# Performance work log

Measured on AMD Instinct MI355X. Metric: run time of the kernel, lower is better.

The kernel has to match this reference:

```python
import jax, jax.numpy as jnp
import numpy as np

B, N, IN_DIM, DIM, HEADS, P = 4, 2048, 256, 512, 8, 16
DH = DIM // HEADS            # 64
SCALE = DH ** -0.5


def setup_inputs() -> dict:
    key = jax.random.key(0)
    ks = jax.random.split(key, 8)
    def w(k, shape, s=0.02):
        return jax.random.normal(k, shape, dtype=jnp.float32) * s
    return {
        "x": jax.random.normal(ks[0], (B, N, IN_DIM), dtype=jnp.float32),
        "w_qkv": w(ks[1], (IN_DIM, 3 * DIM)),
        "b_qkv": jnp.zeros((3 * DIM,), jnp.float32),
        "w_in": w(ks[2], (P, P)),
        "b_in": jnp.zeros((P,), jnp.float32),
        "w_out": w(ks[3], (P, P)),
        "b_out": jnp.zeros((P,), jnp.float32),
        "w_merge": w(ks[4], (DIM, DIM)),
        "b_merge": jnp.zeros((DIM,), jnp.float32),
        "w_proj": w(ks[5], (DIM + IN_DIM, DIM)),
        "b_proj": jnp.zeros((DIM,), jnp.float32),
        "H": 64,
        "W": 32,
    }


def reference(x, w_qkv, b_qkv, w_in, b_in, w_out, b_out,
              w_merge, b_merge, w_proj, b_proj, H, W):
    b, n, _ = x.shape
    qkv = x @ w_qkv + b_qkv                      # [b, n, 3*DIM]
    q, k, v = jnp.split(qkv, 3, axis=-1)
    def to_heads(t):
        return t.reshape(b, n, HEADS, DH).transpose(0, 2, 1, 3)  # [b, h, n, d]
    q, k, v = to_heads(q), to_heads(k), to_heads(v)
    # Original splits heads into h/v halves and runs two attentions, then
    # concats along the head axis. Softmax is per-head, so this is exactly
    # one batched multi-head attention with head order preserved.
    attn = jax.nn.softmax(jnp.einsum('bhnd,bhmd->bhnm', q, k) * SCALE, axis=-1)
    out = jnp.einsum('bhnm,bhmd->bhnd', attn, v)
    out = out.transpose(0, 2, 1, 3).reshape(b, n, DIM)
    out = out @ w_merge + b_merge
    # IBPP branch: view channels as [P, P] grid, linear-SiLU-linear on last dim
    xr = x.reshape(b, n, P, P)
    ib = jax.nn.silu(xr @ w_in + b_in) @ w_out + b_out
    ib = ib.reshape(b, n, IN_DIM)
    # proj (dropout p=0 -> identity)
    return jnp.concatenate([out, ib], axis=-1) @ w_proj + b_proj
```

## Files before the change

### kernel.cpp

```cpp
#include <hip/hip_runtime.h>


typedef unsigned short u16;
typedef unsigned int u32;
typedef __bf16 bf16x8 __attribute__((ext_vector_type(8)));
typedef u16 su16x8 __attribute__((ext_vector_type(8)));
typedef u16 su16x4 __attribute__((ext_vector_type(4)));
typedef u32 u32x4 __attribute__((ext_vector_type(4)));
typedef float f32x4 __attribute__((ext_vector_type(4)));

__device__ __forceinline__ u16 f2bf(float f) {
  union { __bf16 h; u16 u; } v;
  v.h = (__bf16)f;
  return v.u;
}

__device__ __forceinline__ float fexp2(float x) {
#if __has_builtin(__builtin_amdgcn_exp2f)
  return __builtin_amdgcn_exp2f(x);
#else
  return __expf(x * 0.6931471805599453f);
#endif
}

__device__ __forceinline__ f32x4 zero4() {
  f32x4 v = {0.f, 0.f, 0.f, 0.f};
  return v;
}

__device__ __forceinline__ f32x4 mfma16(bf16x8 a, bf16x8 b, f32x4 c) {
  return __builtin_amdgcn_mfma_f32_16x16x32_bf16(a, b, c, 0, 0, 0);
}

__global__ __launch_bounds__(256) void prep_kernel(
    const float* __restrict__ w_qkv, const float* __restrict__ w_merge,
    const float* __restrict__ w_proj, const float* __restrict__ b_merge,
    const float* __restrict__ b_proj, u16* __restrict__ wqkvT,
    u16* __restrict__ wptT, u16* __restrict__ wcombT, u16* __restrict__ wmb,
    float* __restrict__ biasc) {
  int blk = blockIdx.x, tid = threadIdx.x;
  if (blk < 192) {
    const float* src;
    int lsrc, ldd, r0, c0;
    u16* dst;
    if (blk < 96) {
      src = w_qkv; lsrc = 1536; dst = wqkvT; ldd = 256;
      r0 = (blk & 3) * 64; c0 = (blk >> 2) * 64;
    } else if (blk < 160) {
      int b2 = blk - 96;
      src = w_proj; lsrc = 512; dst = wptT; ldd = 512;
      r0 = (b2 & 7) * 64; c0 = (b2 >> 3) * 64;
    } else {
      int b2 = blk - 160;
      src = w_proj + 512 * 512; lsrc = 512; dst = wcombT + 512; ldd = 768;
      r0 = (b2 & 3) * 64; c0 = (b2 >> 2) * 64;
    }
    __shared__ __align__(16) u16 Ts[64 * 68];
    int rr = tid >> 4, cc4 = (tid & 15) * 4;
#pragma unroll
    for (int rep = 0; rep < 4; ++rep) {
      int r = rr + rep * 16;
      float4 v = *(const float4*)&src[(size_t)(r0 + r) * lsrc + c0 + cc4];
      su16x4 pk = {f2bf(v.x), f2bf(v.y), f2bf(v.z), f2bf(v.w)};
      *(su16x4*)&Ts[r * 68 + cc4] = pk;
    }
    __syncthreads();
    int c = tid & 63, seg = tid >> 6;
    u16 tmp[16];
#pragma unroll
    for (int k = 0; k < 16; ++k) tmp[k] = Ts[(seg * 16 + k) * 68 + c];
    *(su16x8*)&dst[(size_t)(c0 + c) * ldd + r0 + seg * 16] = *(su16x8*)tmp;
    *(su16x8*)&dst[(size_t)(c0 + c) * ldd + r0 + seg * 16 + 8] =
        *(su16x8*)(tmp + 8);
  } else if (blk < 256) {
    int b2 = blk - 192;
#pragma unroll
    for (int rep = 0; rep < 4; ++rep) {
      int i = b2 * 4096 + rep * 1024 + tid * 4;
      float4 v = *(const float4*)&w_merge[i];
      su16x4 pk = {f2bf(v.x), f2bf(v.y), f2bf(v.z), f2bf(v.w)};
      *(su16x4*)&wmb[i] = pk;
    }
  } else {
    int col0 = (blk - 256) * 16;
    __shared__ float red[16][17];
    int kr = tid >> 4, cc = tid & 15;
    float s = 0.f;
#pragma unroll 4
    for (int j = 0; j < 32; ++j) {
      int k = kr + j * 16;
      s += b_merge[k] * w_proj[(size_t)k * 512 + col0 + cc];
    }
    red[kr][cc] = s;
    __syncthreads();
    if (kr == 0) {
      float a = b_proj[col0 + cc];
#pragma unroll
      for (int t = 0; t < 16; ++t) a += red[t][cc];
      biasc[col0 + cc] = a;
    }
  }
}

__global__ __launch_bounds__(256) void ib_kernel(
    const float* __restrict__ x, const float* __restrict__ w_in,
    const float* __restrict__ b_in, const float* __restrict__ w_out,
    const float* __restrict__ b_out, u16* __restrict__ xb,
    u16* __restrict__ catb) {
  __shared__ float wi[256], wo[256], bi[16], bo[16];
  __shared__ float xs[16][260];
  __shared__ float hs[16][260];
  int tid = threadIdx.x;
  wi[tid] = w_in[tid];
  wo[tid] = w_out[tid];
  if (tid < 16) { bi[tid] = b_in[tid]; bo[tid] = b_out[tid]; }
  size_t blkoff = (size_t)blockIdx.x * 4096;
#pragma unroll
  for (int i = 0; i < 4; ++i) {
    int f = (tid + i * 256) * 4;
    float4 v = *(const float4*)&x[blkoff + f];
    int tok = f >> 8, p = f & 255;
    *(float4*)&xs[tok][p] = v;
    su16x4 pk = {f2bf(v.x), f2bf(v.y), f2bf(v.z), f2bf(v.w)};
    *(su16x4*)&xb[blkoff + f] = pk;
  }
  __syncthreads();
  int t = tid >> 4, p2 = tid & 15;
#pragma unroll
  for (int p1 = 0; p1 < 16; ++p1) {
    float a = bi[p2];
#pragma unroll
    for (int k = 0; k < 16; ++k) a += xs[t][p1 * 16 + k] * wi[k * 16 + p2];
    hs[t][p1 * 16 + p2] = a / (1.f + __expf(-a));
  }
  __syncthreads();
  size_t tok = (size_t)blockIdx.x * 16 + t;
#pragma unroll
  for (int p1 = 0; p1 < 16; ++p1) {
    float o = bo[p2];
#pragma unroll
    for (int j = 0; j < 16; ++j) o += hs[t][p1 * 16 + j] * wo[j * 16 + p2];
    catb[tok * 768 + 512 + p1 * 16 + p2] = f2bf(o);
  }
}

template <int TM, int TN, int WGM, int WGN, int OUTMODE>
__global__ __launch_bounds__(256) void gemm_bt(
    const u16* __restrict__ A, int lda, const u16* __restrict__ BT, int ldb,
    int kcount, const float* __restrict__ bias, void* __restrict__ Co, int ldc,
    int scaleQ) {
  constexpr int NROWS = TM + TN;
  constexpr int NLD = NROWS / 64;
  constexpr int MT = TM / WGM / 16;
  constexpr int NT = TN / WGN / 16;
  __shared__ __align__(16) u16 S[NROWS * 40];
  int tid = threadIdx.x;
  int lane = tid & 63, wave = tid >> 6;
  int c = lane & 15, g4 = lane >> 4;
  int m0 = blockIdx.y * TM, n0 = blockIdx.x * TN;
  int wm = (wave / WGN) * (TM / WGM), wn = (wave % WGN) * (TN / WGN);
  f32x4 acc[MT][NT];
#pragma unroll
  for (int a = 0; a < MT; ++a)
#pragma unroll
    for (int b = 0; b < NT; ++b) acc[a][b] = zero4();

  su16x8 pre[NLD];
#pragma unroll
  for (int t = 0; t < NLD; ++t) {
    int gsl = t * 256 + tid;
    int row = gsl >> 2, kg = gsl & 3;
    const u16* p = row < TM ? &A[(size_t)(m0 + row) * lda + kg * 8]
                            : &BT[(size_t)(n0 + row - TM) * ldb + kg * 8];
    pre[t] = *(const su16x8*)p;
  }

  for (int kb = 0; kb < kcount; kb += 32) {
    __syncthreads();
#pragma unroll
    for (int t = 0; t < NLD; ++t) {
      int gsl = t * 256 + tid;
      int row = gsl >> 2, kg = gsl & 3;
      *(su16x8*)&S[row * 40 + kg * 8] = pre[t];
    }
    __syncthreads();
    if (kb + 32 < kcount) {
#pragma unroll
      for (int t = 0; t < NLD; ++t) {
        int gsl = t * 256 + tid;
        int row = gsl >> 2, kg = gsl & 3;
        const u16* p =
            row < TM ? &A[(size_t)(m0 + row) * lda + kb + 32 + kg * 8]
                     : &BT[(size_t)(n0 + row - TM) * ldb + kb + 32 + kg * 8];
        pre[t] = *(const su16x8*)p;
      }
    }
    bf16x8 af[MT], bf[NT];
#pragma unroll
    for (int mt = 0; mt < MT; ++mt)
      af[mt] = *(const bf16x8*)&S[(wm + mt * 16 + c) * 40 + g4 * 8];
#pragma unroll
    for (int nt = 0; nt < NT; ++nt)
      bf[nt] = *(const bf16x8*)&S[(TM + wn + nt * 16 + c) * 40 + g4 * 8];
#pragma unroll
    for (int mt = 0; mt < MT; ++mt)
#pragma unroll
      for (int nt = 0; nt < NT; ++nt)
        acc[mt][nt] = mfma16(af[mt], bf[nt], acc[mt][nt]);
  }

  if (OUTMODE == 0) {
    float* Cf = (float*)Co;
#pragma unroll
    for (int nt = 0; nt < NT; ++nt) {
      int col = n0 + wn + nt * 16 + c;
      float bv = bias ? bias[col] : 0.f;
#pragma unroll
      for (int mt = 0; mt < MT; ++mt)
#pragma unroll
        for (int i = 0; i < 4; ++i)
          Cf[(size_t)(m0 + wm + mt * 16 + g4 * 4 + i) * ldc + col] =
              acc[mt][nt][i] + bv;
    }
  } else if (OUTMODE == 2) {
    u16* C16 = (u16*)Co;
#pragma unroll
    for (int nt = 0; nt < NT; ++nt)
#pragma unroll
      for (int mt = 0; mt < MT; ++mt)
#pragma unroll
        for (int i = 0; i < 4; ++i)
          C16[(size_t)(m0 + wm + mt * 16 + g4 * 4 + i) * ldc + n0 + wn +
              nt * 16 + c] = f2bf(acc[mt][nt][i]);
  } else {
    u16* C16 = (u16*)Co;
    u16* Cs = S;
    __syncthreads();
#pragma unroll
    for (int half = 0; half < 2; ++half) {
      if ((wave >> 1) == half) {
#pragma unroll
        for (int nt = 0; nt < NT; ++nt) {
          int col = n0 + wn + nt * 16 + c;
          float bv = bias ? bias[col] : 0.f;
          float sc = (scaleQ && col < 512) ? 0.18033688011112042f : 1.f;
#pragma unroll
          for (int mt = 0; mt < MT; ++mt)
#pragma unroll
            for (int i = 0; i < 4; ++i)
              Cs[(mt * 16 + g4 * 4 + i) * 136 + wn + nt * 16 + c] =
                  f2bf((acc[mt][nt][i] + bv) * sc);
        }
      }
      __syncthreads();
      {
        int row = tid >> 2;
#pragma unroll
        for (int t = 0; t < 4; ++t) {
          int gr = (tid & 3) + t * 4;
          u32x4 v = *(const u32x4*)&Cs[row * 136 + gr * 8];
          *(u32x4*)&C16[(size_t)(m0 + half * 64 + row) * ldc + n0 + gr * 8] = v;
        }
      }
      __syncthreads();
    }
  }
}

__global__ __launch_bounds__(256) void attn_kernel(
    const u16* __restrict__ qkvb, u16* __restrict__ catb) {
  __shared__ __align__(16) u16 Ks[9216];
  __shared__ __align__(16) u16 Vs[8704];
  __shared__ __align__(16) u16 Ps[8704];
  int tid = threadIdx.x;
  int lane = tid & 63, wave = tid >> 6;
  int c = lane & 15, g4 = lane >> 4;
  int wq = wave * 32;
  int bh = blockIdx.x & 31, qt = blockIdx.x >> 5;
  int bb = bh >> 3, h = bh & 7;
  size_t base = (size_t)bb * 2048 * 1536;
  u16* Psw = Ps + wave * (16 * 136);

  bf16x8 qf[2][2];
#pragma unroll
  for (int qt2 = 0; qt2 < 2; ++qt2)
#pragma unroll
    for (int ks2 = 0; ks2 < 2; ++ks2) {
      int n = qt * 128 + wq + qt2 * 16 + c;
      qf[qt2][ks2] = *(const bf16x8*)&qkvb[base + (size_t)n * 1536 + h * 64 +
                                           ks2 * 32 + g4 * 8];
    }
  f32x4 oacc[2][4];
#pragma unroll
  for (int a = 0; a < 2; ++a)
#pragma unroll
    for (int b = 0; b < 4; ++b) oacc[a][b] = zero4();
  float lsum[2] = {0.f, 0.f};

  su16x8 kpre[4], v0pre[2], v1pre[2];
  int kv_s = tid >> 3, dg_s = tid & 7;

  auto loadKV = [&](int n0k) {
#pragma unroll
    for (int t = 0; t < 4; ++t)
      kpre[t] = *(const su16x8*)&qkvb[base + (size_t)(n0k + kv_s + t * 32) *
                                                1536 +
                                      512 + h * 64 + dg_s * 8];
#pragma unroll
    for (int t = 0; t < 2; ++t) {
      const u16* vg = &qkvb[base + (size_t)(n0k + (kv_s + t * 32) * 2) * 1536 +
                            1024 + h * 64 + dg_s * 8];
      v0pre[t] = *(const su16x8*)vg;
      v1pre[t] = *(const su16x8*)(vg + 1536);
    }
  };

  loadKV(0);
  for (int kb2 = 0; kb2 < 16; ++kb2) {
    __syncthreads();
#pragma unroll
    for (int t = 0; t < 4; ++t)
      *(su16x8*)&Ks[(kv_s + t * 32) * 72 + dg_s * 8] = kpre[t];
#pragma unroll
    for (int t = 0; t < 2; ++t) {
      int kvp = kv_s + t * 32;
      u32* vw = (u32*)Vs;
      int kvg = kvp >> 2, w2 = kvp & 3;
#pragma unroll
      for (int j = 0; j < 8; ++j) {
        int d = dg_s * 8 + j;
        vw[d * 68 + ((kvg ^ (dg_s & 3)) << 2) + w2] =
            (u32)v0pre[t][j] | ((u32)v1pre[t][j] << 16);
      }
    }
    __syncthreads();
    if (kb2 < 15) loadKV((kb2 + 1) * 128);
    f32x4 sacc[2][8];
#pragma unroll
    for (int a = 0; a < 2; ++a)
#pragma unroll
      for (int b = 0; b < 8; ++b) sacc[a][b] = zero4();
#pragma unroll
    for (int ks2 = 0; ks2 < 2; ++ks2)
#pragma unroll
      for (int kvt = 0; kvt < 8; ++kvt) {
        bf16x8 kf = *(const bf16x8*)&Ks[(kvt * 16 + c) * 72 + ks2 * 32 + g4 * 8];
        sacc[0][kvt] = mfma16(kf, qf[0][ks2], sacc[0][kvt]);
        sacc[1][kvt] = mfma16(kf, qf[1][ks2], sacc[1][kvt]);
      }
    bf16x8 pf[2][4];
#pragma unroll
    for (int qt2 = 0; qt2 < 2; ++qt2) {
      float part = 0.f;
#pragma unroll
      for (int kvt = 0; kvt < 8; ++kvt) {
        float p0 = fexp2(sacc[qt2][kvt][0]);
        float p1 = fexp2(sacc[qt2][kvt][1]);
        float p2 = fexp2(sacc[qt2][kvt][2]);
        float p3 = fexp2(sacc[qt2][kvt][3]);
        part += (p0 + p1) + (p2 + p3);
        su16x4 pk = {f2bf(p0), f2bf(p1), f2bf(p2), f2bf(p3)};
        *(su16x4*)&Psw[c * 136 + kvt * 16 + g4 * 4] = pk;
      }
      lsum[qt2] += part;
#pragma unroll
      for (int ks = 0; ks < 4; ++ks)
        pf[qt2][ks] = *(const bf16x8*)&Psw[c * 136 + ks * 32 + g4 * 8];
    }
#pragma unroll
    for (int ks = 0; ks < 4; ++ks)
#pragma unroll
      for (int nt = 0; nt < 4; ++nt) {
        int d = nt * 16 + c;
        bf16x8 vf = *(const bf16x8*)&Vs[d * 136 +
                                        (((ks * 4 + g4) ^ ((d >> 3) & 3)) << 3)];
        oacc[0][nt] = mfma16(pf[0][ks], vf, oacc[0][nt]);
        oacc[1][nt] = mfma16(pf[1][ks], vf, oacc[1][nt]);
      }
  }
#pragma unroll
  for (int qt2 = 0; qt2 < 2; ++qt2) {
    lsum[qt2] += __shfl_xor(lsum[qt2], 16);
    lsum[qt2] += __shfl_xor(lsum[qt2], 32);
  }
#pragma unroll
  for (int qt2 = 0; qt2 < 2; ++qt2) {
    float linv[4];
#pragma unroll
    for (int i = 0; i < 4; ++i)
      linv[i] = 1.f / __shfl(lsum[qt2], g4 * 4 + i);
#pragma unroll
    for (int nt = 0; nt < 4; ++nt)
#pragma unroll
      for (int i = 0; i < 4; ++i) {
        int n = qt * 128 + wq + qt2 * 16 + g4 * 4 + i;
        catb[(size_t)(bb * 2048 + n) * 768 + h * 64 + nt * 16 + c] =
            f2bf(oacc[qt2][nt][i] * linv[i]);
      }
  }
}

extern "C" void kernel_launch(void* const* d_in, const int* in_sizes, int n_in,
                              void* d_out, int out_size, void* d_ws,
                              size_t ws_size, hipStream_t stream) {
  const float* x = (const float*)d_in[0];
  const float* w_qkv = (const float*)d_in[1];
  const float* b_qkv = (const float*)d_in[2];
  const float* w_in = (const float*)d_in[3];
  const float* b_in = (const float*)d_in[4];
  const float* w_out = (const float*)d_in[5];
  const float* b_out = (const float*)d_in[6];
  const float* w_merge = (const float*)d_in[7];
  const float* b_merge = (const float*)d_in[8];
  const float* w_proj = (const float*)d_in[9];
  const float* b_proj = (const float*)d_in[10];

  char* ws = (char*)d_ws;
  u16* xb = (u16*)(ws + 0);
  u16* qkvb = (u16*)(ws + 4194304);
  u16* catb = (u16*)(ws + 29360128);
  u16* wqkvT = (u16*)(ws + 41943040);
  u16* wptT = (u16*)(ws + 42729472);
  u16* wmb = (u16*)(ws + 43253760);
  u16* wcombT = (u16*)(ws + 43778048);
  float* biasc = (float*)(ws + 44564480);

  prep_kernel<<<288, 256, 0, stream>>>(w_qkv, w_merge, w_proj, b_merge, b_proj,
                                       wqkvT, wptT, wcombT, wmb, biasc);
  ib_kernel<<<512, 256, 0, stream>>>(x, w_in, b_in, w_out, b_out, xb, catb);
  gemm_bt<128, 128, 2, 2, 1><<<dim3(12, 64), 256, 0, stream>>>(
      xb, 256, wqkvT, 256, 256, b_qkv, (void*)qkvb, 1536, 1);
  gemm_bt<64, 64, 2, 2, 2><<<dim3(8, 8), 256, 0, stream>>>(
      wptT, 512, wmb, 512, 512, nullptr, (void*)wcombT, 768, 0);
  attn_kernel<<<512, 256, 0, stream>>>(qkvb, catb);
  gemm_bt<128, 64, 4, 1, 0><<<dim3(8, 64), 256, 0, stream>>>(
      catb, 768, wcombT, 768, 768, biasc, d_out, 512, 0);
}
```

Baseline: 190.6 us.

## Fuse prep kernels, add async LDS double buffering, pre-transpose V, split attention KV

```diff
diff --git a/kernel.cpp b/kernel.cpp
--- a/kernel.cpp
+++ b/kernel.cpp
@@ -32,30 +32,77 @@
   return __builtin_amdgcn_mfma_f32_16x16x32_bf16(a, b, c, 0, 0, 0);
 }
 
-__global__ __launch_bounds__(256) void prep_kernel(
-    const float* __restrict__ w_qkv, const float* __restrict__ w_merge,
-    const float* __restrict__ w_proj, const float* __restrict__ b_merge,
-    const float* __restrict__ b_proj, u16* __restrict__ wqkvT,
-    u16* __restrict__ wptT, u16* __restrict__ wcombT, u16* __restrict__ wmb,
-    float* __restrict__ biasc) {
+#define GLDS(gp, lp)                                             \
+  __builtin_amdgcn_global_load_lds(                              \
+      (const __attribute__((address_space(1))) u32*)(gp),        \
+      (__attribute__((address_space(3))) u32*)(lp), 16, 0, 0)
+
+__global__ __launch_bounds__(256) void fused_prep(
+    const float* __restrict__ x, const float* __restrict__ w_qkv,
+    const float* __restrict__ w_merge, const float* __restrict__ w_proj,
+    const float* __restrict__ b_merge, const float* __restrict__ b_proj,
+    const float* __restrict__ w_in, const float* __restrict__ b_in,
+    const float* __restrict__ w_out, const float* __restrict__ b_out,
+    u16* __restrict__ wqkvT, u16* __restrict__ wcombT,
+    float* __restrict__ biasc, u16* __restrict__ xb, u16* __restrict__ catb) {
+  __shared__ __align__(16) char SM[35456];
   int blk = blockIdx.x, tid = threadIdx.x;
-  if (blk < 192) {
+  if (blk >= 224) {
+    float* wi = (float*)SM;
+    float* wo = wi + 256;
+    float* bi = wo + 256;
+    float* bo = bi + 16;
+    float* xs = (float*)(SM + 2176);
+    float* hs = (float*)(SM + 18816);
+    int b2 = blk - 224;
+    wi[tid] = w_in[tid];
+    wo[tid] = w_out[tid];
+    if (tid < 16) { bi[tid] = b_in[tid]; bo[tid] = b_out[tid]; }
+    size_t blkoff = (size_t)b2 * 4096;
+#pragma unroll
+    for (int i = 0; i < 4; ++i) {
+      int f = (tid + i * 256) * 4;
+      float4 v = *(const float4*)&x[blkoff + f];
+      int tok = f >> 8, p = f & 255;
+      *(float4*)&xs[tok * 260 + p] = v;
+      su16x4 pk = {f2bf(v.x), f2bf(v.y), f2bf(v.z), f2bf(v.w)};
+      *(su16x4*)&xb[blkoff + f] = pk;
+    }
+    __syncthreads();
+    int t = tid >> 4, p2 = tid & 15;
+#pragma unroll
+    for (int p1 = 0; p1 < 16; ++p1) {
+      float a = bi[p2];
+#pragma unroll
+      for (int k = 0; k < 16; ++k)
+        a += xs[t * 260 + p1 * 16 + k] * wi[k * 16 + p2];
+      hs[t * 260 + p1 * 16 + p2] = a / (1.f + __expf(-a));
+    }
+    __syncthreads();
+    size_t tok = (size_t)b2 * 16 + t;
+#pragma unroll
+    for (int p1 = 0; p1 < 16; ++p1) {
+      float o = bo[p2];
+#pragma unroll
+      for (int j = 0; j < 16; ++j)
+        o += hs[t * 260 + p1 * 16 + j] * wo[j * 16 + p2];
+      catb[tok * 768 + 512 + p1 * 16 + p2] = f2bf(o);
+    }
+    return;
+  }
+  if (blk < 128) {
     const float* src;
     int lsrc, ldd, r0, c0;
     u16* dst;
     if (blk < 96) {
       src = w_qkv; lsrc = 1536; dst = wqkvT; ldd = 256;
       r0 = (blk & 3) * 64; c0 = (blk >> 2) * 64;
-    } else if (blk < 160) {
+    } else {
       int b2 = blk - 96;
-      src = w_proj; lsrc = 512; dst = wptT; ldd = 512;
-      r0 = (b2 & 7) * 64; c0 = (b2 >> 3) * 64;
-    } else {
-      int b2 = blk - 160;
       src = w_proj + 512 * 512; lsrc = 512; dst = wcombT + 512; ldd = 768;
       r0 = (b2 & 3) * 64; c0 = (b2 >> 2) * 64;
     }
-    __shared__ __align__(16) u16 Ts[64 * 68];
+    u16* Ts = (u16*)SM;
     int rr = tid >> 4, cc4 = (tid & 15) * 4;
 #pragma unroll
     for (int rep = 0; rep < 4; ++rep) {
@@ -66,24 +113,76 @@
     }
     __syncthreads();
     int c = tid & 63, seg = tid >> 6;
-    u16 tmp[16];
+    __align__(16) u16 tmp[16];
 #pragma unroll
     for (int k = 0; k < 16; ++k) tmp[k] = Ts[(seg * 16 + k) * 68 + c];
     *(su16x8*)&dst[(size_t)(c0 + c) * ldd + r0 + seg * 16] = *(su16x8*)tmp;
     *(su16x8*)&dst[(size_t)(c0 + c) * ldd + r0 + seg * 16 + 8] =
         *(su16x8*)(tmp + 8);
-  } else if (blk < 256) {
-    int b2 = blk - 192;
-#pragma unroll
-    for (int rep = 0; rep < 4; ++rep) {
-      int i = b2 * 4096 + rep * 1024 + tid * 4;
-      float4 v = *(const float4*)&w_merge[i];
-      su16x4 pk = {f2bf(v.x), f2bf(v.y), f2bf(v.z), f2bf(v.w)};
-      *(su16x4*)&wmb[i] = pk;
-    }
+  } else if (blk < 192) {
+    int b2 = blk - 128;
+    int n0 = (b2 & 7) * 64, m0 = (b2 >> 3) * 64;
+    u16* As = (u16*)SM;
+    u16* Bs = (u16*)(SM + 5120);
+    int lane = tid & 63, wave = tid >> 6;
+    int c = lane & 15, g4 = lane >> 4;
+    int wm = (wave >> 1) * 32, wn = (wave & 1) * 32;
+    f32x4 acc2[2][2];
+#pragma unroll
+    for (int a = 0; a < 2; ++a)
+#pragma unroll
+      for (int b = 0; b < 2; ++b) acc2[a][b] = zero4();
+    for (int k0 = 0; k0 < 512; k0 += 32) {
+      __syncthreads();
+      {
+        int kk = tid >> 3, nn0 = (tid & 7) * 8;
+        const float* sp = &w_proj[(size_t)(k0 + kk) * 512 + n0 + nn0];
+        float4 v0 = *(const float4*)sp;
+        float4 v1 = *(const float4*)(sp + 4);
+        As[(nn0 + 0) * 40 + kk] = f2bf(v0.x);
+        As[(nn0 + 1) * 40 + kk] = f2bf(v0.y);
+        As[(nn0 + 2) * 40 + kk] = f2bf(v0.z);
+        As[(nn0 + 3) * 40 + kk] = f2bf(v0.w);
+        As[(nn0 + 4) * 40 + kk] = f2bf(v1.x);
+        As[(nn0 + 5) * 40 + kk] = f2bf(v1.y);
+        As[(nn0 + 6) * 40 + kk] = f2bf(v1.z);
+        As[(nn0 + 7) * 40 + kk] = f2bf(v1.w);
+      }
+      {
+        int mm = tid >> 2, kk0 = (tid & 3) * 8;
+        const float* sp = &w_merge[(size_t)(m0 + mm) * 512 + k0 + kk0];
+        float4 v0 = *(const float4*)sp;
+        float4 v1 = *(const float4*)(sp + 4);
+        su16x4 p0 = {f2bf(v0.x), f2bf(v0.y), f2bf(v0.z), f2bf(v0.w)};
+        su16x4 p1 = {f2bf(v1.x), f2bf(v1.y), f2bf(v1.z), f2bf(v1.w)};
+        *(su16x4*)&Bs[mm * 40 + kk0] = p0;
+        *(su16x4*)&Bs[mm * 40 + kk0 + 4] = p1;
+      }
+      __syncthreads();
+      bf16x8 af[2], bf[2];
+#pragma unroll
+      for (int mt = 0; mt < 2; ++mt)
+        af[mt] = *(const bf16x8*)&As[(wm + mt * 16 + c) * 40 + g4 * 8];
+#pragma unroll
+      for (int nt = 0; nt < 2; ++nt)
+        bf[nt] = *(const bf16x8*)&Bs[(wn + nt * 16 + c) * 40 + g4 * 8];
+#pragma unroll
+      for (int mt = 0; mt < 2; ++mt)
+#pragma unroll
+        for (int nt = 0; nt < 2; ++nt)
+          acc2[mt][nt] = mfma16(af[mt], bf[nt], acc2[mt][nt]);
+    }
+#pragma unroll
+    for (int mt = 0; mt < 2; ++mt)
+#pragma unroll
+      for (int nt = 0; nt < 2; ++nt)
+#pragma unroll
+        for (int i = 0; i < 4; ++i)
+          wcombT[(size_t)(n0 + wm + mt * 16 + g4 * 4 + i) * 768 + m0 + wn +
+                 nt * 16 + c] = f2bf(acc2[mt][nt][i]);
   } else {
-    int col0 = (blk - 256) * 16;
-    __shared__ float red[16][17];
+    int col0 = (blk - 192) * 16;
+    float* red = (float*)SM;
     int kr = tid >> 4, cc = tid & 15;
     float s = 0.f;
 #pragma unroll 4
@@ -91,147 +190,90 @@
       int k = kr + j * 16;
       s += b_merge[k] * w_proj[(size_t)k * 512 + col0 + cc];
     }
-    red[kr][cc] = s;
+    red[kr * 17 + cc] = s;
     __syncthreads();
     if (kr == 0) {
       float a = b_proj[col0 + cc];
 #pragma unroll
-      for (int t = 0; t < 16; ++t) a += red[t][cc];
+      for (int t = 0; t < 16; ++t) a += red[t * 17 + cc];
       biasc[col0 + cc] = a;
     }
   }
 }
 
-__global__ __launch_bounds__(256) void ib_kernel(
-    const float* __restrict__ x, const float* __restrict__ w_in,
-    const float* __restrict__ b_in, const float* __restrict__ w_out,
-    const float* __restrict__ b_out, u16* __restrict__ xb,
-    u16* __restrict__ catb) {
-  __shared__ float wi[256], wo[256], bi[16], bo[16];
-  __shared__ float xs[16][260];
-  __shared__ float hs[16][260];
-  int tid = threadIdx.x;
-  wi[tid] = w_in[tid];
-  wo[tid] = w_out[tid];
-  if (tid < 16) { bi[tid] = b_in[tid]; bo[tid] = b_out[tid]; }
-  size_t blkoff = (size_t)blockIdx.x * 4096;
-#pragma unroll
-  for (int i = 0; i < 4; ++i) {
-    int f = (tid + i * 256) * 4;
-    float4 v = *(const float4*)&x[blkoff + f];
-    int tok = f >> 8, p = f & 255;
-    *(float4*)&xs[tok][p] = v;
-    su16x4 pk = {f2bf(v.x), f2bf(v.y), f2bf(v.z), f2bf(v.w)};
-    *(su16x4*)&xb[blkoff + f] = pk;
-  }
-  __syncthreads();
-  int t = tid >> 4, p2 = tid & 15;
-#pragma unroll
-  for (int p1 = 0; p1 < 16; ++p1) {
-    float a = bi[p2];
-#pragma unroll
-    for (int k = 0; k < 16; ++k) a += xs[t][p1 * 16 + k] * wi[k * 16 + p2];
-    hs[t][p1 * 16 + p2] = a / (1.f + __expf(-a));
-  }
-  __syncthreads();
-  size_t tok = (size_t)blockIdx.x * 16 + t;
-#pragma unroll
-  for (int p1 = 0; p1 < 16; ++p1) {
-    float o = bo[p2];
-#pragma unroll
-    for (int j = 0; j < 16; ++j) o += hs[t][p1 * 16 + j] * wo[j * 16 + p2];
-    catb[tok * 768 + 512 + p1 * 16 + p2] = f2bf(o);
-  }
-}
-
-template <int TM, int TN, int WGM, int WGN, int OUTMODE>
-__global__ __launch_bounds__(256) void gemm_bt(
+template <int OUTMODE>
+__global__ __launch_bounds__(256, 3) void gemm64(
     const u16* __restrict__ A, int lda, const u16* __restrict__ BT, int ldb,
     int kcount, const float* __restrict__ bias, void* __restrict__ Co, int ldc,
-    int scaleQ) {
-  constexpr int NROWS = TM + TN;
-  constexpr int NLD = NROWS / 64;
-  constexpr int MT = TM / WGM / 16;
-  constexpr int NT = TN / WGN / 16;
-  __shared__ __align__(16) u16 S[NROWS * 40];
-  int tid = threadIdx.x;
-  int lane = tid & 63, wave = tid >> 6;
+    u16* __restrict__ vTout) {
+  constexpr int TM = 128, TN = 64;
+  constexpr int ROWS = TM + TN;
+  constexpr int BUFU = ROWS * 64;
+  __shared__ __align__(16) u16 S[2 * BUFU];
+  int tid = threadIdx.x, lane = tid & 63, wave = tid >> 6;
   int c = lane & 15, g4 = lane >> 4;
   int m0 = blockIdx.y * TM, n0 = blockIdx.x * TN;
-  int wm = (wave / WGN) * (TM / WGM), wn = (wave % WGN) * (TN / WGN);
-  f32x4 acc[MT][NT];
-#pragma unroll
-  for (int a = 0; a < MT; ++a)
-#pragma unroll
-    for (int b = 0; b < NT; ++b) acc[a][b] = zero4();
-
-  su16x8 pre[NLD];
-#pragma unroll
-  for (int t = 0; t < NLD; ++t) {
-    int gsl = t * 256 + tid;
-    int row = gsl >> 2, kg = gsl & 3;
-    const u16* p = row < TM ? &A[(size_t)(m0 + row) * lda + kg * 8]
-                            : &BT[(size_t)(n0 + row - TM) * ldb + kg * 8];
-    pre[t] = *(const su16x8*)p;
-  }
-
-  for (int kb = 0; kb < kcount; kb += 32) {
-    __syncthreads();
-#pragma unroll
-    for (int t = 0; t < NLD; ++t) {
-      int gsl = t * 256 + tid;
-      int row = gsl >> 2, kg = gsl & 3;
-      *(su16x8*)&S[row * 40 + kg * 8] = pre[t];
-    }
-    __syncthreads();
-    if (kb + 32 < kcount) {
-#pragma unroll
-      for (int t = 0; t < NLD; ++t) {
-        int gsl = t * 256 + tid;
-        int row = gsl >> 2, kg = gsl & 3;
-        const u16* p =
-            row < TM ? &A[(size_t)(m0 + row) * lda + kb + 32 + kg * 8]
-                     : &BT[(size_t)(n0 + row - TM) * ldb + kb + 32 + kg * 8];
-        pre[t] = *(const su16x8*)p;
-      }
-    }
-    bf16x8 af[MT], bf[NT];
-#pragma unroll
-    for (int mt = 0; mt < MT; ++mt)
-      af[mt] = *(const bf16x8*)&S[(wm + mt * 16 + c) * 40 + g4 * 8];
-#pragma unroll
-    for (int nt = 0; nt < NT; ++nt)
-      bf[nt] = *(const bf16x8*)&S[(TM + wn + nt * 16 + c) * 40 + g4 * 8];
-#pragma unroll
-    for (int mt = 0; mt < MT; ++mt)
-#pragma unroll
-      for (int nt = 0; nt < NT; ++nt)
-        acc[mt][nt] = mfma16(af[mt], bf[nt], acc[mt][nt]);
+  int wm = (wave >> 1) * 64, wn = (wave & 1) * 32;
+  int lr = lane >> 3, lg = lane & 7;
+  f32x4 acc[4][2];
+#pragma unroll
+  for (int a = 0; a < 4; ++a)
+#pragma unroll
+    for (int b = 0; b < 2; ++b) acc[a][b] = zero4();
+
+  auto stage = [&](int kb, int bsel) {
+#pragma unroll
+    for (int t = 0; t < 6; ++t) {
+      int chunk = wave * 6 + t;
+      int row = chunk * 8 + lr;
+      int gs = lg ^ lr;
+      const u16* gp = row < TM
+                          ? &A[(size_t)(m0 + row) * lda + kb + gs * 8]
+                          : &BT[(size_t)(n0 + row - TM) * ldb + kb + gs * 8];
+      GLDS(gp, &S[bsel * BUFU + chunk * 512]);
+    }
+  };
+  stage(0, 0);
+  int nIter = kcount >> 6;
+  for (int it = 0; it < nIter; ++it) {
+    int bsel = it & 1;
+    __syncthreads();
+    if (it + 1 < nIter) stage((it + 1) << 6, bsel ^ 1);
+    bf16x8 af[4][2], bf[2][2];
+#pragma unroll
+    for (int ks = 0; ks < 2; ++ks) {
+#pragma unroll
+      for (int mt = 0; mt < 4; ++mt)
+        af[mt][ks] = *(const bf16x8*)&S[bsel * BUFU + (wm + mt * 16 + c) * 64 +
+                                        ((ks * 4 + g4) ^ (c & 7)) * 8];
+#pragma unroll
+      for (int nt = 0; nt < 2; ++nt)
+        bf[nt][ks] =
+            *(const bf16x8*)&S[bsel * BUFU + (TM + wn + nt * 16 + c) * 64 +
+                               ((ks * 4 + g4) ^ (c & 7)) * 8];
+    }
+#pragma unroll
+    for (int ks = 0; ks < 2; ++ks)
+#pragma unroll
+      for (int mt = 0; mt < 4; ++mt)
+#pragma unroll
+        for (int nt = 0; nt < 2; ++nt)
+          acc[mt][nt] = mfma16(af[mt][ks], bf[nt][ks], acc[mt][nt]);
   }
 
   if (OUTMODE == 0) {
     float* Cf = (float*)Co;
 #pragma unroll
-    for (int nt = 0; nt < NT; ++nt) {
+    for (int nt = 0; nt < 2; ++nt) {
       int col = n0 + wn + nt * 16 + c;
       float bv = bias ? bias[col] : 0.f;
 #pragma unroll
-      for (int mt = 0; mt < MT; ++mt)
+      for (int mt = 0; mt < 4; ++mt)
 #pragma unroll
         for (int i = 0; i < 4; ++i)
           Cf[(size_t)(m0 + wm + mt * 16 + g4 * 4 + i) * ldc + col] =
               acc[mt][nt][i] + bv;
     }
-  } else if (OUTMODE == 2) {
-    u16* C16 = (u16*)Co;
-#pragma unroll
-    for (int nt = 0; nt < NT; ++nt)
-#pragma unroll
-      for (int mt = 0; mt < MT; ++mt)
-#pragma unroll
-        for (int i = 0; i < 4; ++i)
-          C16[(size_t)(m0 + wm + mt * 16 + g4 * 4 + i) * ldc + n0 + wn +
-              nt * 16 + c] = f2bf(acc[mt][nt][i]);
   } else {
     u16* C16 = (u16*)Co;
     u16* Cs = S;
@@ -240,163 +282,179 @@
     for (int half = 0; half < 2; ++half) {
       if ((wave >> 1) == half) {
 #pragma unroll
-        for (int nt = 0; nt < NT; ++nt) {
+        for (int nt = 0; nt < 2; ++nt) {
           int col = n0 + wn + nt * 16 + c;
           float bv = bias ? bias[col] : 0.f;
-          float sc = (scaleQ && col < 512) ? 0.18033688011112042f : 1.f;
-#pragma unroll
-          for (int mt = 0; mt < MT; ++mt)
+          float sc = (col < 512) ? 0.18033688011112042f : 1.f;
+#pragma unroll
+          for (int mt = 0; mt < 4; ++mt)
 #pragma unroll
             for (int i = 0; i < 4; ++i)
-              Cs[(mt * 16 + g4 * 4 + i) * 136 + wn + nt * 16 + c] =
+              Cs[(mt * 16 + g4 * 4 + i) * 72 + wn + nt * 16 + c] =
                   f2bf((acc[mt][nt][i] + bv) * sc);
         }
       }
       __syncthreads();
-      {
+      if (n0 < 1024) {
         int row = tid >> 2;
 #pragma unroll
-        for (int t = 0; t < 4; ++t) {
+        for (int t = 0; t < 2; ++t) {
           int gr = (tid & 3) + t * 4;
-          u32x4 v = *(const u32x4*)&Cs[row * 136 + gr * 8];
+          u32x4 v = *(const u32x4*)&Cs[row * 72 + gr * 8];
           *(u32x4*)&C16[(size_t)(m0 + half * 64 + row) * ldc + n0 + gr * 8] = v;
         }
+      } else {
+        int d = tid >> 2, tr = (tid & 3) * 16;
+        __align__(16) u16 tmp[16];
+#pragma unroll
+        for (int j = 0; j < 16; ++j) tmp[j] = Cs[(tr + j) * 72 + d];
+        int b = m0 >> 11, h = (n0 - 1024) >> 6;
+        size_t vaddr = ((size_t)((b * 8 + h) * 64 + d)) * 2048 + (m0 & 2047) +
+                       half * 64 + tr;
+        *(su16x8*)&vTout[vaddr] = *(su16x8*)tmp;
+        *(su16x8*)&vTout[vaddr + 8] = *(su16x8*)(tmp + 8);
       }
       __syncthreads();
     }
   }
 }
 
-__global__ __launch_bounds__(256) void attn_kernel(
-    const u16* __restrict__ qkvb, u16* __restrict__ catb) {
-  __shared__ __align__(16) u16 Ks[9216];
-  __shared__ __align__(16) u16 Vs[8704];
-  __shared__ __align__(16) u16 Ps[8704];
-  int tid = threadIdx.x;
-  int lane = tid & 63, wave = tid >> 6;
+__global__ __launch_bounds__(512, 4) void attn_kernel(
+    const u16* __restrict__ qkb, const u16* __restrict__ vT,
+    u16* __restrict__ catb) {
+  __shared__ __align__(16) u16 SMu[20736];
+  u16* Ks = SMu;
+  u16* Vs = SMu + 8192;
+  u16* Ps = SMu + 16384;
+  int tid = threadIdx.x, lane = tid & 63, wave = tid >> 6;
   int c = lane & 15, g4 = lane >> 4;
-  int wq = wave * 32;
+  int qg = wave >> 1, kvh = wave & 1;
   int bh = blockIdx.x & 31, qt = blockIdx.x >> 5;
   int bb = bh >> 3, h = bh & 7;
-  size_t base = (size_t)bb * 2048 * 1536;
-  u16* Psw = Ps + wave * (16 * 136);
+  size_t kbase = (size_t)bb * 2048 * 1024;
+  size_t vbase = (size_t)((bb * 8 + h) * 64) * 2048;
+  u16* Psw = Ps + wave * 544;
+  int lr = lane >> 3, lg = lane & 7;
+
+  union { su16x8 u; bf16x8 b; } one_;
+#pragma unroll
+  for (int j = 0; j < 8; ++j) one_.u[j] = 0x3F80;
+  bf16x8 onesb = one_.b;
 
   bf16x8 qf[2][2];
 #pragma unroll
-  for (int qt2 = 0; qt2 < 2; ++qt2)
+  for (int qh = 0; qh < 2; ++qh)
 #pragma unroll
     for (int ks2 = 0; ks2 < 2; ++ks2) {
-      int n = qt * 128 + wq + qt2 * 16 + c;
-      qf[qt2][ks2] = *(const bf16x8*)&qkvb[base + (size_t)n * 1536 + h * 64 +
-                                           ks2 * 32 + g4 * 8];
-    }
-  f32x4 oacc[2][4];
-#pragma unroll
-  for (int a = 0; a < 2; ++a)
+      int n = qt * 128 + qg * 32 + qh * 16 + c;
+      qf[qh][ks2] = *(const bf16x8*)&qkb[kbase + (size_t)n * 1024 + h * 64 +
+                                         ks2 * 32 + g4 * 8];
+    }
+  f32x4 oacc[2][4], lacc[2];
+#pragma unroll
+  for (int a = 0; a < 2; ++a) {
+    lacc[a] = zero4();
 #pragma unroll
     for (int b = 0; b < 4; ++b) oacc[a][b] = zero4();
-  float lsum[2] = {0.f, 0.f};
-
-  su16x8 kpre[4], v0pre[2], v1pre[2];
-  int kv_s = tid >> 3, dg_s = tid & 7;
-
-  auto loadKV = [&](int n0k) {
-#pragma unroll
-    for (int t = 0; t < 4; ++t)
-      kpre[t] = *(const su16x8*)&qkvb[base + (size_t)(n0k + kv_s + t * 32) *
-                                                1536 +
-                                      512 + h * 64 + dg_s * 8];
-#pragma unroll
-    for (int t = 0; t < 2; ++t) {
-      const u16* vg = &qkvb[base + (size_t)(n0k + (kv_s + t * 32) * 2) * 1536 +
-                            1024 + h * 64 + dg_s * 8];
-      v0pre[t] = *(const su16x8*)vg;
-      v1pre[t] = *(const su16x8*)(vg + 1536);
-    }
+  }
+
+  auto stageK = [&](int n0k, int bsel) {
+    int kv = wave * 8 + lr;
+    const u16* gp = &qkb[kbase + (size_t)(n0k + kv) * 1024 + 512 + h * 64 +
+                         (lg ^ lr) * 8];
+    GLDS(gp, &Ks[bsel * 4096 + wave * 512]);
   };
-
-  loadKV(0);
-  for (int kb2 = 0; kb2 < 16; ++kb2) {
-    __syncthreads();
-#pragma unroll
-    for (int t = 0; t < 4; ++t)
-      *(su16x8*)&Ks[(kv_s + t * 32) * 72 + dg_s * 8] = kpre[t];
-#pragma unroll
-    for (int t = 0; t < 2; ++t) {
-      int kvp = kv_s + t * 32;
-      u32* vw = (u32*)Vs;
-      int kvg = kvp >> 2, w2 = kvp & 3;
-#pragma unroll
-      for (int j = 0; j < 8; ++j) {
-        int d = dg_s * 8 + j;
-        vw[d * 68 + ((kvg ^ (dg_s & 3)) << 2) + w2] =
-            (u32)v0pre[t][j] | ((u32)v1pre[t][j] << 16);
-      }
-    }
-    __syncthreads();
-    if (kb2 < 15) loadKV((kb2 + 1) * 128);
-    f32x4 sacc[2][8];
+  auto stageV = [&](int n0k, int bsel) {
+    int d = wave * 8 + lr;
+    const u16* gp = &vT[vbase + (size_t)d * 2048 + n0k + (lg ^ lr) * 8];
+    GLDS(gp, &Vs[bsel * 4096 + wave * 512]);
+  };
+  stageK(0, 0);
+  stageV(0, 0);
+
+  for (int it = 0; it < 32; ++it) {
+    int bsel = it & 1;
+    __syncthreads();
+    if (it < 31) {
+      stageK((it + 1) * 64, bsel ^ 1);
+      stageV((it + 1) * 64, bsel ^ 1);
+    }
+    f32x4 sacc[2][2];
 #pragma unroll
     for (int a = 0; a < 2; ++a)
 #pragma unroll
-      for (int b = 0; b < 8; ++b) sacc[a][b] = zero4();
+      for (int b = 0; b < 2; ++b) sacc[a][b] = zero4();
 #pragma unroll
     for (int ks2 = 0; ks2 < 2; ++ks2)
 #pragma unroll
-      for (int kvt = 0; kvt < 8; ++kvt) {
-        bf16x8 kf = *(const bf16x8*)&Ks[(kvt * 16 + c) * 72 + ks2 * 32 + g4 * 8];
+      for (int kvt = 0; kvt < 2; ++kvt) {
+        bf16x8 kf = *(const bf16x8*)&Ks[bsel * 4096 +
+                                        (kvh * 32 + kvt * 16 + c) * 64 +
+                                        ((ks2 * 4 + g4) ^ (c & 7)) * 8];
         sacc[0][kvt] = mfma16(kf, qf[0][ks2], sacc[0][kvt]);
         sacc[1][kvt] = mfma16(kf, qf[1][ks2], sacc[1][kvt]);
       }
-    bf16x8 pf[2][4];
-#pragma unroll
-    for (int qt2 = 0; qt2 < 2; ++qt2) {
-      float part = 0.f;
-#pragma unroll
-      for (int kvt = 0; kvt < 8; ++kvt) {
-        float p0 = fexp2(sacc[qt2][kvt][0]);
-        float p1 = fexp2(sacc[qt2][kvt][1]);
-        float p2 = fexp2(sacc[qt2][kvt][2]);
-        float p3 = fexp2(sacc[qt2][kvt][3]);
-        part += (p0 + p1) + (p2 + p3);
+    bf16x8 pf[2];
+#pragma unroll
+    for (int qh = 0; qh < 2; ++qh) {
+#pragma unroll
+      for (int kvt = 0; kvt < 2; ++kvt) {
+        float p0 = fexp2(sacc[qh][kvt][0]);
+        float p1 = fexp2(sacc[qh][kvt][1]);
+        float p2 = fexp2(sacc[qh][kvt][2]);
+        float p3 = fexp2(sacc[qh][kvt][3]);
         su16x4 pk = {f2bf(p0), f2bf(p1), f2bf(p2), f2bf(p3)};
-        *(su16x4*)&Psw[c * 136 + kvt * 16 + g4 * 4] = pk;
-      }
-      lsum[qt2] += part;
-#pragma unroll
-      for (int ks = 0; ks < 4; ++ks)
-        pf[qt2][ks] = *(const bf16x8*)&Psw[c * 136 + ks * 32 + g4 * 8];
-    }
-#pragma unroll
-    for (int ks = 0; ks < 4; ++ks)
-#pragma unroll
-      for (int nt = 0; nt < 4; ++nt) {
-        int d = nt * 16 + c;
-        bf16x8 vf = *(const bf16x8*)&Vs[d * 136 +
-                                        (((ks * 4 + g4) ^ ((d >> 3) & 3)) << 3)];
-        oacc[0][nt] = mfma16(pf[0][ks], vf, oacc[0][nt]);
-        oacc[1][nt] = mfma16(pf[1][ks], vf, oacc[1][nt]);
-      }
-  }
-#pragma unroll
-  for (int qt2 = 0; qt2 < 2; ++qt2) {
-    lsum[qt2] += __shfl_xor(lsum[qt2], 16);
-    lsum[qt2] += __shfl_xor(lsum[qt2], 32);
-  }
-#pragma unroll
-  for (int qt2 = 0; qt2 < 2; ++qt2) {
-    float linv[4];
-#pragma unroll
-    for (int i = 0; i < 4; ++i)
-      linv[i] = 1.f / __shfl(lsum[qt2], g4 * 4 + i);
-#pragma unroll
-    for (int nt = 0; nt < 4; ++nt)
-#pragma unroll
-      for (int i = 0; i < 4; ++i) {
-        int n = qt * 128 + wq + qt2 * 16 + g4 * 4 + i;
-        catb[(size_t)(bb * 2048 + n) * 768 + h * 64 + nt * 16 + c] =
-            f2bf(oacc[qt2][nt][i] * linv[i]);
-      }
+        *(su16x4*)&Psw[c * 34 + kvt * 16 + g4 * 4] = pk;
+      }
+      pf[qh] = *(const bf16x8*)&Psw[c * 34 + g4 * 8];
+      lacc[qh] = mfma16(pf[qh], onesb, lacc[qh]);
+    }
+#pragma unroll
+    for (int nt = 0; nt < 4; ++nt) {
+      int d = nt * 16 + c;
+      bf16x8 vf = *(const bf16x8*)&Vs[bsel * 4096 + d * 64 +
+                                      ((kvh * 4 + g4) ^ (c & 7)) * 8];
+      oacc[0][nt] = mfma16(pf[0], vf, oacc[0][nt]);
+      oacc[1][nt] = mfma16(pf[1], vf, oacc[1][nt]);
+    }
+  }
+
+  __syncthreads();
+  float* ob = (float*)SMu;
+  float* lb = (float*)(SMu + 17408);
+  if (kvh == 1) {
+#pragma unroll
+    for (int qh = 0; qh < 2; ++qh) {
+      int qr = qg * 32 + qh * 16 + g4 * 4;
+#pragma unroll
+      for (int nt = 0; nt < 4; ++nt)
+#pragma unroll
+        for (int i = 0; i < 4; ++i)
+          ob[(qr + i) * 68 + nt * 16 + c] = oacc[qh][nt][i];
+      if (c == 0)
+#pragma unroll
+        for (int i = 0; i < 4; ++i) lb[qr + i] = lacc[qh][i];
+    }
+  }
+  __syncthreads();
+  if (kvh == 0) {
+#pragma unroll
+    for (int qh = 0; qh < 2; ++qh) {
+      int qr = qg * 32 + qh * 16 + g4 * 4;
+      float linv[4];
+#pragma unroll
+      for (int i = 0; i < 4; ++i)
+        linv[i] = 1.f / (lacc[qh][i] + lb[qr + i]);
+#pragma unroll
+      for (int nt = 0; nt < 4; ++nt)
+#pragma unroll
+        for (int i = 0; i < 4; ++i) {
+          int n = qt * 128 + qr + i;
+          catb[(size_t)(bb * 2048 + n) * 768 + h * 64 + nt * 16 + c] =
+              f2bf((oacc[qh][nt][i] + ob[(qr + i) * 68 + nt * 16 + c]) *
+                   linv[i]);
+        }
+    }
   }
 }
 
@@ -417,22 +475,19 @@
 
   char* ws = (char*)d_ws;
   u16* xb = (u16*)(ws + 0);
-  u16* qkvb = (u16*)(ws + 4194304);
+  u16* qkb = (u16*)(ws + 4194304);
+  u16* vT = (u16*)(ws + 20971520);
   u16* catb = (u16*)(ws + 29360128);
   u16* wqkvT = (u16*)(ws + 41943040);
-  u16* wptT = (u16*)(ws + 42729472);
-  u16* wmb = (u16*)(ws + 43253760);
-  u16* wcombT = (u16*)(ws + 43778048);
-  float* biasc = (float*)(ws + 44564480);
-
-  prep_kernel<<<288, 256, 0, stream>>>(w_qkv, w_merge, w_proj, b_merge, b_proj,
-                                       wqkvT, wptT, wcombT, wmb, biasc);
-  ib_kernel<<<512, 256, 0, stream>>>(x, w_in, b_in, w_out, b_out, xb, catb);
-  gemm_bt<128, 128, 2, 2, 1><<<dim3(12, 64), 256, 0, stream>>>(
-      xb, 256, wqkvT, 256, 256, b_qkv, (void*)qkvb, 1536, 1);
-  gemm_bt<64, 64, 2, 2, 2><<<dim3(8, 8), 256, 0, stream>>>(
-      wptT, 512, wmb, 512, 512, nullptr, (void*)wcombT, 768, 0);
-  attn_kernel<<<512, 256, 0, stream>>>(qkvb, catb);
-  gemm_bt<128, 64, 4, 1, 0><<<dim3(8, 64), 256, 0, stream>>>(
-      catb, 768, wcombT, 768, 768, biasc, d_out, 512, 0);
-}
+  u16* wcombT = (u16*)(ws + 42729472);
+  float* biasc = (float*)(ws + 43515904);
+
+  fused_prep<<<736, 256, 0, stream>>>(x, w_qkv, w_merge, w_proj, b_merge,
+                                      b_proj, w_in, b_in, w_out, b_out, wqkvT,
+                                      wcombT, biasc, xb, catb);
+  gemm64<1><<<dim3(24, 64), 256, 0, stream>>>(xb, 256, wqkvT, 256, 256, b_qkv,
+                                              (void*)qkb, 1024, vT);
+  attn_kernel<<<512, 512, 0, stream>>>(qkb, vT, catb);
+  gemm64<0><<<dim3(8, 64), 256, 0, stream>>>(catb, 768, wcombT, 768, 768,
+                                             biasc, d_out, 512, nullptr);
+}
```

Result: slower. 240.5 us (+26.2%).
